# Kernel optimization log

Measured on AMD Instinct MI355X. Metric: run time of the kernel, lower is better.

Reference implementation:

```python
import jax, jax.numpy as jnp
import numpy as np

B, N, D_IN, D_OUT, H, W = 2, 2048, 1024, 1024, 16, 64
DH = D_OUT // H


def setup_inputs() -> dict:
    key = jax.random.key(0)
    ks = jax.random.split(key, 6)
    x = jax.random.normal(ks[0], (B, N, D_IN), dtype=jnp.float32)
    s_in = 1.0 / np.sqrt(D_IN)
    s_out = 1.0 / np.sqrt(D_OUT)
    wq = jax.random.normal(ks[1], (D_IN, D_OUT), dtype=jnp.float32) * s_in
    wk = jax.random.normal(ks[2], (D_IN, D_OUT), dtype=jnp.float32) * s_in
    wv = jax.random.normal(ks[3], (D_IN, D_OUT), dtype=jnp.float32) * s_in
    wo = jax.random.normal(ks[4], (D_OUT, D_OUT), dtype=jnp.float32) * s_out
    # sparse global tokens: every 256th token is global
    global_attention = (jnp.arange(N)[None, :] % 256 == 0) & jnp.ones((B, 1), bool)
    return {"x": x, "wq": wq, "wk": wk, "wv": wv, "wo": wo,
            "global_attention": global_attention}


def _mask(global_attention):
    # True = masked out. Causal local window + global rows/cols unmasked.
    i = jnp.arange(N)[:, None]
    j = jnp.arange(N)[None, :]
    allowed = (i - j < W) & (i >= j)          # causal sliding window
    local_mask = ~allowed                      # [N, N], True = masked
    g = global_attention                       # [B, N] bool
    # global token j clears row j and column j of the mask
    global_clear = g[:, :, None] | g[:, None, :]   # [B, N, N]
    return local_mask[None, :, :] & ~global_clear  # [B, N, N]


def reference(x, wq, wk, wv, wo, global_attention):
    b, n, _ = x.shape
    q = (x @ wq).reshape(b, n, H, DH).transpose(0, 2, 1, 3)  # [b,h,n,dh]
    k = (x @ wk).reshape(b, n, H, DH).transpose(0, 2, 1, 3)
    v = (x @ wv).reshape(b, n, H, DH).transpose(0, 2, 1, 3)
    scores = jnp.einsum('bhqd,bhkd->bhqk', q, k) / jnp.sqrt(jnp.float32(DH))
    mask = _mask(global_attention)[:, None, :, :]            # [b,1,n,n]
    scores = jnp.where(mask, -jnp.inf, scores)
    attn = jax.nn.softmax(scores, axis=-1)
    ctx = jnp.einsum('bhqk,bhkd->bqhd', attn, v).reshape(b, n, D_OUT)
    return ctx @ wo
```

## Files before the change

### kernel.cpp

```cpp
#include <hip/hip_runtime.h>


using u16 = unsigned short;
using u32 = unsigned int;

typedef __attribute__((ext_vector_type(8))) short bf16x8;
typedef __attribute__((ext_vector_type(4))) float f32x4;

__device__ __forceinline__ float b2f(u16 s) {
  union { u32 u; float f; } x; x.u = ((u32)s) << 16; return x.f;
}
__device__ __forceinline__ u16 f2b(float f) {
  union { float f; u32 u; } x; x.f = f;
  u32 r = (x.u + 0x7fffu + ((x.u >> 16) & 1u)) >> 16;
  return (u16)r;
}
__device__ __forceinline__ u32 cvtpk(float lo, float hi) {
  u32 r; asm("v_cvt_pk_bf16_f32 %0, %1, %2" : "=v"(r) : "v"(lo), "v"(hi)); return r;
}

__global__ __launch_bounds__(256) void k_pre(const float* __restrict__ wq,
                                             const float* __restrict__ wk,
                                             const float* __restrict__ wv,
                                             const float* __restrict__ wo,
                                             u16* __restrict__ wqkvT,
                                             u16* __restrict__ woT) {
  __shared__ float tile[64][65];
  const int id = blockIdx.x;
  const int z = id >> 8, xy = id & 255;
  const float* src = (z == 0) ? wq : (z == 1) ? wk : (z == 2) ? wv : wo;
  u16* dst = (z < 3) ? (wqkvT + ((size_t)z << 20)) : woT;
  const int n0 = (xy & 15) * 64, k0 = (xy >> 4) * 64;
  const int tx = threadIdx.x & 63, ty = threadIdx.x >> 6;
  #pragma unroll
  for (int r = 0; r < 64; r += 4)
    tile[r + ty][tx] = src[(size_t)(k0 + r + ty) * 1024 + n0 + tx];
  __syncthreads();
  #pragma unroll
  for (int r = 0; r < 64; r += 4)
    dst[(size_t)(n0 + r + ty) * 1024 + k0 + tx] = f2b(tile[tx][r + ty]);
}

__device__ __forceinline__ void gload16(const u16* g, u16* l) {
  __builtin_amdgcn_global_load_lds((const __attribute__((address_space(1))) void*)g,
                                   (__attribute__((address_space(3))) void*)l, 16, 0, 0);
}

__global__ __launch_bounds__(256, 3) void k_qkv(const float* __restrict__ X,
                                                const u16* __restrict__ Bt,
                                                u16* __restrict__ C) {
  __shared__ u16 lds[3][2][4096];
  const int K = 1024, N = 3072, NT = 32;
  const int t = threadIdx.x;
  const int wid = t >> 6, lane = t & 63;
  const int l4 = lane >> 4, l16 = lane & 15;
  const int wr = wid >> 1, wc = wid & 1;
  const int d = blockIdx.y * gridDim.x + blockIdx.x;
  const int qq = (gridDim.x * gridDim.y) >> 3;
  const int tau = (d & 7) * qq + (d >> 3);
  const int bn = tau % gridDim.x, bm = tau / gridDim.x;
  const float* Ax = X + (size_t)bm * 128 * K;
  const u16* Bb = Bt + (size_t)bn * 128 * K;
  const int srow0 = t >> 2;
  const int scol = (((t & 3) ^ ((t >> 3) & 3)) << 3);
  const int sdst = wid << 9;
  const int adst = (wid << 9) + (lane << 3);
  const int sl8 = ((l4 ^ ((l16 >> 1) & 3)) << 3);
  f32x4 acc[4][4] = {};
  float4 fa0[2][2], fa1[2][2];

  int c0 = 0, c1 = 1, c2 = 2;

  #define QKV_ISSUE(FA, BUF, KT)                                                  \
    { const int k0_ = (KT) << 5;                                                  \
      _Pragma("unroll")                                                           \
      for (int c = 0; c < 2; ++c) {                                               \
        const float* ap = Ax + (size_t)(c * 64 + srow0) * K + k0_ + scol;         \
        FA[c][0] = *(const float4*)ap;                                            \
        FA[c][1] = *(const float4*)(ap + 4);                                      \
        gload16(Bb + (size_t)(c * 64 + srow0) * K + k0_ + scol,                   \
                &lds[BUF][1][c * 2048 + sdst]);                                   \
      } }

  #define QKV_WRITE(FA, BUF)                                                      \
    { _Pragma("unroll")                                                           \
      for (int c = 0; c < 2; ++c) {                                               \
        union { u32 w[4]; uint4 v; } u_;                                          \
        u_.w[0] = cvtpk(FA[c][0].x, FA[c][0].y);                                  \
        u_.w[1] = cvtpk(FA[c][0].z, FA[c][0].w);                                  \
        u_.w[2] = cvtpk(FA[c][1].x, FA[c][1].y);                                  \
        u_.w[3] = cvtpk(FA[c][1].z, FA[c][1].w);                                  \
        *(uint4*)&lds[BUF][0][c * 2048 + adst] = u_.v;                            \
      } }

  #define QKV_COMPUTE(BUF)                                                        \
    { const u16* As = lds[BUF][0];                                                \
      const u16* Bs = lds[BUF][1];                                                \
      bf16x8 af[4], bf[4];                                                        \
      _Pragma("unroll")                                                           \
      for (int m = 0; m < 4; ++m)                                                 \
        af[m] = *(const bf16x8*)&As[(wr * 64 + m * 16 + l16) * 32 + sl8];         \
      _Pragma("unroll")                                                           \
      for (int n = 0; n < 4; ++n)                                                 \
        bf[n] = *(const bf16x8*)&Bs[(wc * 64 + n * 16 + l16) * 32 + sl8];         \
      __builtin_amdgcn_s_setprio(1);                                              \
      _Pragma("unroll")                                                           \
      for (int m = 0; m < 4; ++m)                                                 \
        _Pragma("unroll")                                                         \
        for (int n = 0; n < 4; ++n)                                               \
          acc[m][n] = __builtin_amdgcn_mfma_f32_16x16x32_bf16(af[m], bf[n],       \
                                                              acc[m][n], 0, 0, 0);\
      __builtin_amdgcn_s_setprio(0); }

  QKV_ISSUE(fa0, 0, 0);
  QKV_ISSUE(fa1, 1, 1);
  QKV_WRITE(fa0, 0);
  asm volatile("s_waitcnt vmcnt(6)" ::: "memory");
  asm volatile("s_waitcnt lgkmcnt(0)" ::: "memory");
  __builtin_amdgcn_s_barrier();

  for (int tt = 0; tt < NT; tt += 2) {
    QKV_WRITE(fa1, c1);
    if (tt + 2 < NT) QKV_ISSUE(fa0, c2, tt + 2);
    QKV_COMPUTE(c0);
    if (tt + 2 < NT) asm volatile("s_waitcnt vmcnt(6)" ::: "memory");
    else             asm volatile("s_waitcnt vmcnt(0)" ::: "memory");
    asm volatile("s_waitcnt lgkmcnt(0)" ::: "memory");
    __builtin_amdgcn_s_barrier();
    { int tmp = c0; c0 = c1; c1 = c2; c2 = tmp; }
    if (tt + 2 < NT) QKV_WRITE(fa0, c1);
    if (tt + 3 < NT) QKV_ISSUE(fa1, c2, tt + 3);
    QKV_COMPUTE(c0);
    if (tt + 2 < NT) {
      if (tt + 3 < NT) asm volatile("s_waitcnt vmcnt(6)" ::: "memory");
      else             asm volatile("s_waitcnt vmcnt(0)" ::: "memory");
      asm volatile("s_waitcnt lgkmcnt(0)" ::: "memory");
      __builtin_amdgcn_s_barrier();
      { int tmp = c0; c0 = c1; c1 = c2; c2 = tmp; }
    }
  }
  #undef QKV_ISSUE
  #undef QKV_WRITE
  #undef QKV_COMPUTE

  #pragma unroll
  for (int m = 0; m < 4; ++m) {
    const int row0 = bm * 128 + wr * 64 + m * 16 + l4 * 4;
    #pragma unroll
    for (int n = 0; n < 4; ++n) {
      const int col = bn * 128 + wc * 64 + n * 16 + l16;
      #pragma unroll
      for (int r = 0; r < 4; ++r)
        C[(size_t)(row0 + r) * N + col] = f2b(acc[m][n][r]);
    }
  }
}

template<int F32OUT, int GRED>
__global__ __launch_bounds__(256, 2) void k_gemm64(const u16* __restrict__ A,
                                                   const u16* __restrict__ Bt,
                                                   void* __restrict__ C, int N, int K,
                                                   const float* __restrict__ gpart,
                                                   u16* __restrict__ ctxw) {
  __shared__ u16 lds[3][6144];
  const int t = threadIdx.x;
  const int wid = t >> 6, lane = t & 63;
  const int l4 = lane >> 4, l16 = lane & 15;
  const int wr = wid >> 1, wc = wid & 1;
  const int d = blockIdx.y * gridDim.x + blockIdx.x;
  const int qq = (gridDim.x * gridDim.y) >> 3;
  const int tau = (d & 7) * qq + (d >> 3);
  const int bn = tau % gridDim.x, bm = tau / gridDim.x;
  const u16* Ab = A + (size_t)bm * 64 * K;
  const u16* Bb = Bt + (size_t)bn * 128 * K;
  const int srow0 = t >> 2;
  const int scol = (((t & 3) ^ ((t >> 3) & 3)) << 3);
  const int sdst = wid << 9;
  const int sl8 = ((l4 ^ ((l16 >> 1) & 3)) << 3);
  const int NT = K >> 5;
  f32x4 acc[2][4] = {};

  if (GRED && (bm & 3) == 0) {
    const int bb = bm >> 5;
    const int irow = (bm & 31) * 64;
    const int row8 = (bm & 31) >> 2;
    const int h = t >> 4;
    const int d0 = (t & 15) * 4;
    const float* g0 = gpart + ((size_t)(bb * 16 + h) * 32) * 520;
    float o0 = 0.f, o1 = 0.f, o2 = 0.f, o3 = 0.f, ls = 0.f;
    for (int q = 0; q < 32; ++q) {
      const float4 v = *(const float4*)(g0 + q * 520 + row8 * 64 + d0);
      o0 += v.x; o1 += v.y; o2 += v.z; o3 += v.w;
      ls += g0[q * 520 + 512 + row8];
    }
    const float inv = 1.f / ls;
    u16* cw = ctxw + ((size_t)(bb * 2048 + irow)) * 1024 + h * 64 + d0;
    cw[0] = f2b(o0 * inv); cw[1] = f2b(o1 * inv);
    cw[2] = f2b(o2 * inv); cw[3] = f2b(o3 * inv);
    __syncthreads();
  }

  #pragma unroll
  for (int pt = 0; pt < 2; ++pt) {
    gload16(Ab + (size_t)srow0 * K + (pt << 5) + scol, &lds[pt][sdst]);
    #pragma unroll
    for (int c = 0; c < 2; ++c)
      gload16(Bb + (size_t)(c * 64 + srow0) * K + (pt << 5) + scol,
              &lds[pt][2048 + c * 2048 + sdst]);
  }

  int cur = 0, nxt2 = 2;
  for (int tt = 0; tt < NT; ++tt) {
    if (tt + 1 < NT) asm volatile("s_waitcnt vmcnt(3)" ::: "memory");
    else             asm volatile("s_waitcnt vmcnt(0)" ::: "memory");
    __builtin_amdgcn_s_barrier();
    if (tt + 2 < NT) {
      const int k0 = (tt + 2) << 5;
      u16* dst = &lds[nxt2][0];
      gload16(Ab + (size_t)srow0 * K + k0 + scol, dst + sdst);
      #pragma unroll
      for (int c = 0; c < 2; ++c)
        gload16(Bb + (size_t)(c * 64 + srow0) * K + k0 + scol, dst + 2048 + c * 2048 + sdst);
    }
    const u16* As = lds[cur];
    const u16* Bs = lds[cur] + 2048;
    bf16x8 af[2], bf[4];
    #pragma unroll
    for (int m = 0; m < 2; ++m)
      af[m] = *(const bf16x8*)&As[(wr * 32 + m * 16 + l16) * 32 + sl8];
    #pragma unroll
    for (int n = 0; n < 4; ++n)
      bf[n] = *(const bf16x8*)&Bs[(wc * 64 + n * 16 + l16) * 32 + sl8];
    __builtin_amdgcn_s_setprio(1);
    #pragma unroll
    for (int m = 0; m < 2; ++m)
      #pragma unroll
      for (int n = 0; n < 4; ++n)
        acc[m][n] = __builtin_amdgcn_mfma_f32_16x16x32_bf16(af[m], bf[n], acc[m][n], 0, 0, 0);
    __builtin_amdgcn_s_setprio(0);
    cur = (cur == 2) ? 0 : cur + 1;
    nxt2 = (nxt2 == 2) ? 0 : nxt2 + 1;
  }

  #pragma unroll
  for (int m = 0; m < 2; ++m) {
    const int row0 = bm * 64 + wr * 32 + m * 16 + l4 * 4;
    #pragma unroll
    for (int n = 0; n < 4; ++n) {
      const int col = bn * 128 + wc * 64 + n * 16 + l16;
      #pragma unroll
      for (int r = 0; r < 4; ++r) {
        if (F32OUT) ((float*)C)[(size_t)(row0 + r) * N + col] = acc[m][n][r];
        else        ((u16*)C)[(size_t)(row0 + r) * N + col] = f2b(acc[m][n][r]);
      }
    }
  }
}

__global__ __launch_bounds__(256) void k_attn_tile(const u16* __restrict__ qkv,
                                                   u16* __restrict__ ctx,
                                                   float* __restrict__ gpart) {
  __shared__ u16 buf[26880];
  __shared__ u16 Qgs[16 * 72];
  __shared__ u16 Pgs[16 * 72];
  __shared__ float lred[4][16];
  u16* Qs = buf;
  u16* Ks = buf + 4608;
  u16* Vt = buf + 16128;
  u16* Ps = buf;

  const int t = threadIdx.x, wid = t >> 6, lane = t & 63;
  const int l4 = lane >> 4, l16 = lane & 15;
  const int qt = blockIdx.x, h = blockIdx.y, b = blockIdx.z;
  const int q0 = qt * 64;
  const int kbase = q0 - 64;
  const size_t base = (size_t)b * 2048 * 3072;
  const u16* Qg = qkv + base + h * 64;
  const u16* Kg = qkv + base + 1024 + h * 64;
  const u16* Vg = qkv + base + 2048 + h * 64;

  for (int s = t; s < 512; s += 256) {
    int r = s >> 3, c = (s & 7) * 8;
    *(uint4*)&Qs[r * 72 + c] = *(const uint4*)&Qg[(size_t)(q0 + r) * 3072 + c];
  }
  if (t < 128) {
    int r = t >> 3, c = (t & 7) * 8;
    if (r < 8) {
      *(uint4*)&Qgs[r * 72 + c] = *(const uint4*)&Qg[(size_t)(r * 256) * 3072 + c];
    } else {
      uint4 z = {0, 0, 0, 0};
      *(uint4*)&Qgs[r * 72 + c] = z;
    }
  }
  for (int s = t; s < 1088; s += 256) {
    int r = s >> 3, c = (s & 7) * 8;
    int j = (r < 128) ? max(kbase + r, 0) : (r - 128) * 256;
    *(uint4*)&Ks[r * 72 + c] = *(const uint4*)&Kg[(size_t)j * 3072 + c];
  }
  for (int s = t; s < 1088; s += 256) {
    int r = s >> 3, c = (s & 7) * 8;
    int j = (r < 128) ? max(kbase + r, 0) : (r - 128) * 256;
    uint4 v = *(const uint4*)&Vg[(size_t)j * 3072 + c];
    const u16* pv = (const u16*)&v;
    const int ch = r >> 3;
    #pragma unroll
    for (int e8 = 0; e8 < 8; ++e8) {
      const int d = c + e8;
      const int kd = ((d >> 3) ^ d) & 7;
      const int chs = (ch < 16) ? (ch ^ kd) : ch;
      Vt[d * 168 + chs * 8 + (r & 7)] = pv[e8];
    }
  }
  for (int z = t; z < 64 * 24; z += 256) {
    int d = z / 24, j = 136 + z % 24;
    Vt[d * 168 + j] = 0;
  }
  __syncthreads();

  f32x4 sa[10] = {};
  #pragma unroll
  for (int ks = 0; ks < 2; ++ks) {
    bf16x8 qa = *(const bf16x8*)&Qs[(wid * 16 + l16) * 72 + ks * 32 + l4 * 8];
    #pragma unroll
    for (int n = 0; n < 10; ++n) {
      bf16x8 kb = *(const bf16x8*)&Ks[(n * 16 + l16) * 72 + ks * 32 + l4 * 8];
      sa[n] = __builtin_amdgcn_mfma_f32_16x16x32_bf16(qa, kb, sa[n], 0, 0, 0);
    }
  }

  f32x4 sg = {};
  #pragma unroll
  for (int ks = 0; ks < 2; ++ks) {
    bf16x8 qa = *(const bf16x8*)&Qgs[l16 * 72 + ks * 32 + l4 * 8];
    bf16x8 kb = *(const bf16x8*)&Ks[(64 + wid * 16 + l16) * 72 + ks * 32 + l4 * 8];
    sg = __builtin_amdgcn_mfma_f32_16x16x32_bf16(qa, kb, sg, 0, 0, 0);
  }
  #pragma unroll
  for (int r = 0; r < 4; ++r) {
    float p = __expf(sg[r] * 0.125f);
    sg[r] = p;
    #pragma unroll
    for (int o = 1; o < 16; o <<= 1) p += __shfl_xor(p, o);
    if (l16 == 0) lred[wid][l4 * 4 + r] = p;
  }
  #pragma unroll
  for (int r = 0; r < 4; ++r)
    Pgs[(l4 * 4 + r) * 72 + wid * 16 + l16] = f2b(sg[r]);

  const int qi0 = wid * 16 + l4 * 4;
  #pragma unroll
  for (int n = 0; n < 10; ++n) {
    const int jc = n * 16 + l16;
    #pragma unroll
    for (int r = 0; r < 4; ++r) {
      const int qi = qi0 + r;
      bool allowed;
      if (n < 8) {
        const int kr = kbase + jc;
        allowed = (jc > qi) && (jc <= qi + 64) && (kr >= 0) && ((kr & 255) != 0);
      } else {
        allowed = (jc < 136);
      }
      sa[n][r] = allowed ? sa[n][r] * 0.125f : -1e30f;
    }
  }

  float m[4], l[4];
  #pragma unroll
  for (int r = 0; r < 4; ++r) {
    float mx = sa[0][r];
    #pragma unroll
    for (int n = 1; n < 10; ++n) mx = fmaxf(mx, sa[n][r]);
    #pragma unroll
    for (int o = 1; o < 16; o <<= 1) mx = fmaxf(mx, __shfl_xor(mx, o));
    m[r] = mx;
    l[r] = 0.f;
  }
  #pragma unroll
  for (int n = 0; n < 10; ++n)
    #pragma unroll
    for (int r = 0; r < 4; ++r) {
      float p = __expf(sa[n][r] - m[r]);
      sa[n][r] = p;
      l[r] += p;
    }
  #pragma unroll
  for (int r = 0; r < 4; ++r)
    #pragma unroll
    for (int o = 1; o < 16; o <<= 1) l[r] += __shfl_xor(l[r], o);

  __syncthreads();

  u16* Pw = Ps + wid * (16 * 168);
  #pragma unroll
  for (int n = 0; n < 10; ++n)
    #pragma unroll
    for (int r = 0; r < 4; ++r)
      Pw[(l4 * 4 + r) * 168 + n * 16 + l16] = f2b(sa[n][r]);
  __syncthreads();

  f32x4 o[4] = {};
  #pragma unroll
  for (int ks = 0; ks < 5; ++ks) {
    bf16x8 pa = *(const bf16x8*)&Pw[l16 * 168 + ks * 32 + l4 * 8];
    #pragma unroll
    for (int dt = 0; dt < 4; ++dt) {
      const int dvo = dt * 16 + l16;
      const int kdo = ((dvo >> 3) ^ dvo) & 7;
      const int ch = ks * 4 + l4;
      const int chs = (ch < 16) ? (ch ^ kdo) : ch;
      bf16x8 vb = *(const bf16x8*)&Vt[dvo * 168 + chs * 8];
      o[dt] = __builtin_amdgcn_mfma_f32_16x16x32_bf16(pa, vb, o[dt], 0, 0, 0);
    }
  }

  f32x4 og = {};
  {
    const int dV = wid * 16 + l16;
    const int kdg = ((dV >> 3) ^ dV) & 7;
    #pragma unroll
    for (int ks = 0; ks < 2; ++ks) {
      bf16x8 pa = *(const bf16x8*)&Pgs[l16 * 72 + ks * 32 + l4 * 8];
      const int chs = (8 + ks * 4 + l4) ^ kdg;
      bf16x8 vb = *(const bf16x8*)&Vt[dV * 168 + chs * 8];
      og = __builtin_amdgcn_mfma_f32_16x16x32_bf16(pa, vb, og, 0, 0, 0);
    }
  }
  float* gp = gpart + ((size_t)(b * 16 + h) * 32 + qt) * 520;
  #pragma unroll
  for (int r = 0; r < 4; ++r) {
    int row = l4 * 4 + r;
    if (row < 8) gp[row * 64 + wid * 16 + l16] = og[r];
  }
  if (t < 8) gp[512 + t] = lred[0][t] + lred[1][t] + lred[2][t] + lred[3][t];

  #pragma unroll
  for (int r = 0; r < 4; ++r) {
    const int q = q0 + qi0 + r;
    if ((q & 255) == 0) continue;
    const float inv = 1.0f / l[r];
    #pragma unroll
    for (int dt = 0; dt < 4; ++dt)
      ctx[(size_t)(b * 2048 + q) * 1024 + h * 64 + dt * 16 + l16] = f2b(o[dt][r] * inv);
  }
}

extern "C" void kernel_launch(void* const* d_in, const int* in_sizes, int n_in,
                              void* d_out, int out_size, void* d_ws, size_t ws_size,
                              hipStream_t stream) {
  (void)in_sizes; (void)n_in; (void)out_size; (void)ws_size;
  const float* x  = (const float*)d_in[0];
  const float* wq = (const float*)d_in[1];
  const float* wk = (const float*)d_in[2];
  const float* wv = (const float*)d_in[3];
  const float* wo = (const float*)d_in[4];
  char* ws = (char*)d_ws;
  u16* qkv   = (u16*)(ws + (8u  << 20));
  u16* ctx   = (u16*)(ws + (32u << 20));
  u16* wqkvT = (u16*)(ws + (40u << 20));
  u16* woT   = (u16*)(ws + (46u << 20));
  float* gpart = (float*)(ws);

  k_pre<<<1024, 256, 0, stream>>>(wq, wk, wv, wo, wqkvT, woT);
  k_qkv<<<dim3(24, 32), 256, 0, stream>>>(x, wqkvT, qkv);
  k_attn_tile<<<dim3(32, 16, 2), 256, 0, stream>>>(qkv, ctx, gpart);
  k_gemm64<1, 1><<<dim3(8, 64), 256, 0, stream>>>(ctx, woT, d_out, 1024, 1024, gpart, ctx);
}
```

Baseline: 89.01 us.

## Deepen QKV GEMM fp32 A-operand prefetch to three register stages

Restructures the k_qkv main loop so fp32 A tiles are prefetched three k-steps ahead in registers (fa0/fa1/fa2), while B tiles still go straight to LDS two steps ahead. The loop is fully unrolled by three with static buffer indices, and sched_barriers fix the order of issue. The aim is to hide global load latency better in the QKV projection GEMM. The cost is more VGPRs for the extra fp32 staging, which could lower occupancy under launch_bounds(256,3).

```diff
diff --git a/kernel.cpp b/kernel.cpp
--- a/kernel.cpp
+++ b/kernel.cpp
@@ -50,7 +50,7 @@
                                                 const u16* __restrict__ Bt,
                                                 u16* __restrict__ C) {
   __shared__ u16 lds[3][2][4096];
-  const int K = 1024, N = 3072, NT = 32;
+  const int K = 1024, N = 3072;
   const int t = threadIdx.x;
   const int wid = t >> 6, lane = t & 63;
   const int l4 = lane >> 4, l16 = lane & 15;
@@ -67,81 +67,106 @@
   const int adst = (wid << 9) + (lane << 3);
   const int sl8 = ((l4 ^ ((l16 >> 1) & 3)) << 3);
   f32x4 acc[4][4] = {};
-  float4 fa0[2][2], fa1[2][2];
-
-  int c0 = 0, c1 = 1, c2 = 2;
-
-  #define QKV_ISSUE(FA, BUF, KT)                                                  \
-    { const int k0_ = (KT) << 5;                                                  \
-      _Pragma("unroll")                                                           \
-      for (int c = 0; c < 2; ++c) {                                               \
-        const float* ap = Ax + (size_t)(c * 64 + srow0) * K + k0_ + scol;         \
-        FA[c][0] = *(const float4*)ap;                                            \
-        FA[c][1] = *(const float4*)(ap + 4);                                      \
-        gload16(Bb + (size_t)(c * 64 + srow0) * K + k0_ + scol,                   \
-                &lds[BUF][1][c * 2048 + sdst]);                                   \
+  float4 fa0[2][2], fa1[2][2], fa2[2][2];
+
+  #define QKV_ISSUE_B(BUF, KT)                                                  \
+    { const int k0_ = (KT) << 5;                                                \
+      _Pragma("unroll")                                                         \
+      for (int c = 0; c < 2; ++c)                                               \
+        gload16(Bb + (size_t)(c * 64 + srow0) * K + k0_ + scol,                 \
+                &lds[BUF][1][c * 2048 + sdst]); }
+
+  #define QKV_ISSUE_A(FA, KT)                                                   \
+    { const int k0_ = (KT) << 5;                                                \
+      _Pragma("unroll")                                                         \
+      for (int c = 0; c < 2; ++c) {                                             \
+        const float* ap = Ax + (size_t)(c * 64 + srow0) * K + k0_ + scol;       \
+        FA[c][0] = *(const float4*)ap;                                          \
+        FA[c][1] = *(const float4*)(ap + 4);                                    \
       } }
 
-  #define QKV_WRITE(FA, BUF)                                                      \
-    { _Pragma("unroll")                                                           \
-      for (int c = 0; c < 2; ++c) {                                               \
-        union { u32 w[4]; uint4 v; } u_;                                          \
-        u_.w[0] = cvtpk(FA[c][0].x, FA[c][0].y);                                  \
-        u_.w[1] = cvtpk(FA[c][0].z, FA[c][0].w);                                  \
-        u_.w[2] = cvtpk(FA[c][1].x, FA[c][1].y);                                  \
-        u_.w[3] = cvtpk(FA[c][1].z, FA[c][1].w);                                  \
-        *(uint4*)&lds[BUF][0][c * 2048 + adst] = u_.v;                            \
+  #define QKV_WRITE(FA, BUF)                                                    \
+    { _Pragma("unroll")                                                         \
+      for (int c = 0; c < 2; ++c) {                                             \
+        union { u32 w[4]; uint4 v; } u_;                                        \
+        u_.w[0] = cvtpk(FA[c][0].x, FA[c][0].y);                                \
+        u_.w[1] = cvtpk(FA[c][0].z, FA[c][0].w);                                \
+        u_.w[2] = cvtpk(FA[c][1].x, FA[c][1].y);                                \
+        u_.w[3] = cvtpk(FA[c][1].z, FA[c][1].w);                                \
+        *(uint4*)&lds[BUF][0][c * 2048 + adst] = u_.v;                          \
       } }
 
-  #define QKV_COMPUTE(BUF)                                                        \
-    { const u16* As = lds[BUF][0];                                                \
-      const u16* Bs = lds[BUF][1];                                                \
-      bf16x8 af[4], bf[4];                                                        \
-      _Pragma("unroll")                                                           \
-      for (int m = 0; m < 4; ++m)                                                 \
-        af[m] = *(const bf16x8*)&As[(wr * 64 + m * 16 + l16) * 32 + sl8];         \
-      _Pragma("unroll")                                                           \
-      for (int n = 0; n < 4; ++n)                                                 \
-        bf[n] = *(const bf16x8*)&Bs[(wc * 64 + n * 16 + l16) * 32 + sl8];         \
-      __builtin_amdgcn_s_setprio(1);                                              \
-      _Pragma("unroll")                                                           \
-      for (int m = 0; m < 4; ++m)                                                 \
-        _Pragma("unroll")                                                         \
-        for (int n = 0; n < 4; ++n)                                               \
-          acc[m][n] = __builtin_amdgcn_mfma_f32_16x16x32_bf16(af[m], bf[n],       \
+  #define QKV_COMPUTE(BUF)                                                      \
+    { const u16* As = lds[BUF][0];                                              \
+      const u16* Bs = lds[BUF][1];                                              \
+      bf16x8 af[4], bf[4];                                                      \
+      _Pragma("unroll")                                                         \
+      for (int m = 0; m < 4; ++m)                                               \
+        af[m] = *(const bf16x8*)&As[(wr * 64 + m * 16 + l16) * 32 + sl8];       \
+      _Pragma("unroll")                                                         \
+      for (int n = 0; n < 4; ++n)                                               \
+        bf[n] = *(const bf16x8*)&Bs[(wc * 64 + n * 16 + l16) * 32 + sl8];       \
+      __builtin_amdgcn_s_setprio(1);                                            \
+      _Pragma("unroll")                                                         \
+      for (int m = 0; m < 4; ++m)                                               \
+        _Pragma("unroll")                                                       \
+        for (int n = 0; n < 4; ++n)                                             \
+          acc[m][n] = __builtin_amdgcn_mfma_f32_16x16x32_bf16(af[m], bf[n],     \
                                                               acc[m][n], 0, 0, 0);\
       __builtin_amdgcn_s_setprio(0); }
 
-  QKV_ISSUE(fa0, 0, 0);
-  QKV_ISSUE(fa1, 1, 1);
+  #define QKV_STEP(TT, FW, BW, BB, FAN, BC, VM)                                 \
+    QKV_WRITE(FW, BW);                                                          \
+    QKV_ISSUE_B(BB, (TT) + 2);                                                  \
+    __builtin_amdgcn_sched_barrier(0);                                          \
+    QKV_ISSUE_A(FAN, (TT) + 3);                                                 \
+    __builtin_amdgcn_sched_barrier(0);                                          \
+    QKV_COMPUTE(BC);                                                            \
+    asm volatile("s_waitcnt vmcnt(" #VM ")" ::: "memory");                      \
+    asm volatile("s_waitcnt lgkmcnt(0)" ::: "memory");                          \
+    __builtin_amdgcn_s_barrier();
+
+  QKV_ISSUE_A(fa0, 0);
+  __builtin_amdgcn_sched_barrier(0);
+  QKV_ISSUE_B(0, 0);
+  __builtin_amdgcn_sched_barrier(0);
+  QKV_ISSUE_A(fa1, 1);
+  __builtin_amdgcn_sched_barrier(0);
+  QKV_ISSUE_B(1, 1);
+  __builtin_amdgcn_sched_barrier(0);
+  QKV_ISSUE_A(fa2, 2);
+  __builtin_amdgcn_sched_barrier(0);
   QKV_WRITE(fa0, 0);
+  asm volatile("s_waitcnt vmcnt(10)" ::: "memory");
+  asm volatile("s_waitcnt lgkmcnt(0)" ::: "memory");
+  __builtin_amdgcn_s_barrier();
+
+  for (int tt = 0; tt < 27; tt += 3) {
+    QKV_STEP(tt + 0, fa1, 1, 2, fa0, 0, 10)
+    QKV_STEP(tt + 1, fa2, 2, 0, fa1, 1, 10)
+    QKV_STEP(tt + 2, fa0, 0, 1, fa2, 2, 10)
+  }
+  QKV_STEP(27, fa1, 1, 2, fa0, 0, 10)
+  QKV_STEP(28, fa2, 2, 0, fa1, 1, 10)
+  QKV_WRITE(fa0, 0);
+  QKV_ISSUE_B(1, 31);
+  __builtin_amdgcn_sched_barrier(0);
+  QKV_COMPUTE(2);
   asm volatile("s_waitcnt vmcnt(6)" ::: "memory");
   asm volatile("s_waitcnt lgkmcnt(0)" ::: "memory");
   __builtin_amdgcn_s_barrier();
-
-  for (int tt = 0; tt < NT; tt += 2) {
-    QKV_WRITE(fa1, c1);
-    if (tt + 2 < NT) QKV_ISSUE(fa0, c2, tt + 2);
-    QKV_COMPUTE(c0);
-    if (tt + 2 < NT) asm volatile("s_waitcnt vmcnt(6)" ::: "memory");
-    else             asm volatile("s_waitcnt vmcnt(0)" ::: "memory");
-    asm volatile("s_waitcnt lgkmcnt(0)" ::: "memory");
-    __builtin_amdgcn_s_barrier();
-    { int tmp = c0; c0 = c1; c1 = c2; c2 = tmp; }
-    if (tt + 2 < NT) QKV_WRITE(fa0, c1);
-    if (tt + 3 < NT) QKV_ISSUE(fa1, c2, tt + 3);
-    QKV_COMPUTE(c0);
-    if (tt + 2 < NT) {
-      if (tt + 3 < NT) asm volatile("s_waitcnt vmcnt(6)" ::: "memory");
-      else             asm volatile("s_waitcnt vmcnt(0)" ::: "memory");
-      asm volatile("s_waitcnt lgkmcnt(0)" ::: "memory");
-      __builtin_amdgcn_s_barrier();
-      { int tmp = c0; c0 = c1; c1 = c2; c2 = tmp; }
-    }
-  }
-  #undef QKV_ISSUE
+  QKV_WRITE(fa1, 1);
+  QKV_COMPUTE(0);
+  asm volatile("s_waitcnt vmcnt(0)" ::: "memory");
+  asm volatile("s_waitcnt lgkmcnt(0)" ::: "memory");
+  __builtin_amdgcn_s_barrier();
+  QKV_COMPUTE(1);
+
+  #undef QKV_ISSUE_B
+  #undef QKV_ISSUE_A
   #undef QKV_WRITE
   #undef QKV_COMPUTE
+  #undef QKV_STEP
 
   #pragma unroll
   for (int m = 0; m < 4; ++m) {
```

After: 88.95 us. About the same (-0.1%).
